# Performance work log

Hardware: AMD Instinct MI355X
Metric: run time of the kernel (lower is better)

Reference implementation:

```python
import jax, jax.numpy as jnp
import numpy as np

TEMPERATURE = 0.07
EPS = 1e-12  # F.normalize eps


def _l2_normalize(x):
    # matches torch F.normalize(dim=1): x / max(||x||, eps)
    n = jnp.linalg.norm(x, axis=1, keepdims=True)
    return x / jnp.maximum(n, EPS)


def setup_inputs() -> dict:
    key = jax.random.key(0)
    k1, k2 = jax.random.split(key)
    N, Z = 4096, 256
    z1 = jax.random.normal(k1, (N, Z), dtype=jnp.float32)
    z2 = jax.random.normal(k2, (N, Z), dtype=jnp.float32)
    return {"z1": z1, "z2": z2}


def reference(z1, z2):
    N = z1.shape[0]
    z1n = _l2_normalize(z1)
    z2n = _l2_normalize(z2)
    reps = jnp.concatenate([z1n, z2n], axis=0)          # [2N, Z]
    sim = reps @ reps.T                                  # cosine sim (rows unit-norm)
    # positives: sim[i, i+N] for i<N and sim[i, i-N] for i>=N
    pos = jnp.concatenate([jnp.diagonal(sim, offset=N),
                           jnp.diagonal(sim, offset=-N)])  # [2N]
    # The row logits are {positive} U {all sims except self and positive},
    # i.e. all entries except the self-similarity diagonal.
    inv_t = 1.0 / TEMPERATURE
    twoN = 2 * N
    diag_mask = jnp.eye(twoN, dtype=bool)
    logits = jnp.where(diag_mask, -jnp.inf, sim * inv_t)   # [2N, 2N]
    lse = jax.nn.logsumexp(logits, axis=1)                 # [2N]
    # cross_entropy with label at the positive: -pos/T + lse, sum / 2N
    loss = jnp.mean(lse - pos * inv_t)
    return loss
```

## Files before the change

### kernel.cpp

```cpp
#include <hip/hip_runtime.h>
#include <hip/hip_bf16.h>

#define N_ROWS 4096
#define TWO_N  8192
#define ZDIM   256
#define INV_T  (1.0f/0.07f)
#define EXP_SCALE (INV_T * 1.44269504088896340736f)

typedef __attribute__((ext_vector_type(4))) float f32x4;
typedef __attribute__((ext_vector_type(8))) int   i32x8;
typedef __attribute__((ext_vector_type(2))) int   i32x2;

#define SCALE_ONE 0x7F7F7F7F

__device__ __forceinline__ void async_load16(const void* g, void* lds_uniform_base) {
  __builtin_amdgcn_global_load_lds(
      (const __attribute__((address_space(1))) void*)g,
      (__attribute__((address_space(3))) void*)lds_uniform_base, 16, 0, 0);
}

__device__ __forceinline__ unsigned char f32_to_e4m3(float x) {
  unsigned int u = __float_as_uint(x);
  const unsigned int s = u >> 31;
  unsigned int a = u & 0x7FFFFFFFu;
  if (a > 0x43E00000u) a = 0x43E00000u;
  const float f = __uint_as_float(a);
  unsigned int out;
  if (a < (121u << 23)) {
    const int m = (int)rintf(f * 512.0f);
    out = (unsigned int)m;
  } else {
    const unsigned int r = a + 0x7FFFFu + ((a >> 20) & 1u);
    const unsigned int e8 = (r >> 23) - 120u;
    out = (e8 << 3) | ((r >> 20) & 7u);
  }
  return (unsigned char)(out | (s << 7));
}

__global__ __launch_bounds__(256) void normalize_kernel(
    const float* __restrict__ z1, const float* __restrict__ z2,
    unsigned char* __restrict__ reps, float* __restrict__ pos,
    float* __restrict__ out) {
  const int lane = threadIdx.x & 63;
  const int wave = threadIdx.x >> 6;
  const int r = blockIdx.x * 4 + wave;
  const float4 a = ((const float4*)(z1 + (size_t)r * ZDIM))[lane];
  const float4 b = ((const float4*)(z2 + (size_t)r * ZDIM))[lane];
  float s1 = a.x*a.x + a.y*a.y + a.z*a.z + a.w*a.w;
  float s2 = b.x*b.x + b.y*b.y + b.z*b.z + b.w*b.w;
  float s3 = a.x*b.x + a.y*b.y + a.z*b.z + a.w*b.w;
  #pragma unroll
  for (int m = 1; m < 64; m <<= 1) {
    s1 += __shfl_xor(s1, m, 64);
    s2 += __shfl_xor(s2, m, 64);
    s3 += __shfl_xor(s3, m, 64);
  }
  const float inv1 = 1.0f / fmaxf(sqrtf(s1), 1e-12f);
  const float inv2 = 1.0f / fmaxf(sqrtf(s2), 1e-12f);
  uchar4 pa, pb;
  pa.x = f32_to_e4m3(a.x * inv1); pa.y = f32_to_e4m3(a.y * inv1);
  pa.z = f32_to_e4m3(a.z * inv1); pa.w = f32_to_e4m3(a.w * inv1);
  pb.x = f32_to_e4m3(b.x * inv2); pb.y = f32_to_e4m3(b.y * inv2);
  pb.z = f32_to_e4m3(b.z * inv2); pb.w = f32_to_e4m3(b.w * inv2);
  ((uchar4*)(reps + (size_t)r * ZDIM))[lane] = pa;
  ((uchar4*)(reps + (size_t)(r + N_ROWS) * ZDIM))[lane] = pb;
  if (lane == 0) {
    pos[r] = s3 * inv1 * inv2;
    if (r == 0) out[0] = INV_T;
  }
}

__global__ __launch_bounds__(256, 2) void simsum_kernel(
    const unsigned char* __restrict__ reps,
    float* __restrict__ rowscratch,
    float* __restrict__ colscratch) {
  __shared__ __align__(16) unsigned char Alds[128 * 256];
  __shared__ __align__(16) unsigned char Blds[2][128 * 128];
  __shared__ float colred[2][256];

  const int tid  = threadIdx.x;
  const int lane = tid & 63;
  const int wave = tid >> 6;
  const int wm = wave >> 1, wn = wave & 1;
  const int quad = lane >> 4;
  const int l16  = lane & 15;
  const int itile = blockIdx.x;
  const int chunk = blockIdx.y;
  const int rowBase = itile * 128;
  const char* gbase = (const char*)reps;
  const bool diaghere = (chunk == 0);

  {
    const int r0 = tid >> 4;
    const int src = (tid & 8) | ((tid ^ (tid >> 4)) & 7);
    const char* g0 = gbase + (rowBase + r0) * ZDIM + src * 16;
    char* l0 = (char*)Alds + (wave << 10);
    #pragma unroll
    for (int p = 0; p < 8; ++p)
      async_load16(g0 + p * 16 * ZDIM, l0 + p * 4096);
  }

  int doff[4];
  int noff;
  if (diaghere) {
    doff[0] = 1; doff[1] = 2; doff[2] = 3; doff[3] = 32;
    noff = (itile < 32) ? 4 : 3;
  } else {
    doff[0] = chunk * 4; doff[1] = chunk * 4 + 1;
    doff[2] = chunk * 4 + 2; doff[3] = chunk * 4 + 3;
    noff = 4;
  }
  const int Q = noff * 2;

#define STAGE_B(q_) do {                                                        \
    const int t_ = (q_) >> 1, c_ = (q_) & 1;                                    \
    const int jt_ = (itile + doff[t_]) & 63;                                    \
    const int r0_ = tid >> 3;                                        \
    const int src_ = (tid ^ (tid >> 3)) & 7;                                    \
    const char* g0_ = gbase + (jt_ * 128 + r0_) * ZDIM + c_ * 128 + src_ * 16;  \
    char* l0_ = (char*)Blds[c_] + (wave << 10);                                 \
    _Pragma("unroll")                                                           \
    for (int p_ = 0; p_ < 4; ++p_)                                              \
      async_load16(g0_ + p_ * 32 * ZDIM, l0_ + p_ * 4096);                      \
  } while (0)

  float rowpart[16];
  #pragma unroll
  for (int i = 0; i < 16; ++i) rowpart[i] = 0.0f;
  const f32x4 zero4 = {0.0f, 0.0f, 0.0f, 0.0f};

  if (diaghere) {
    __syncthreads();
    if (Q > 0) STAGE_B(0);
    f32x4 acc[4][4];
    #pragma unroll
    for (int mi = 0; mi < 4; ++mi)
      #pragma unroll
      for (int ni = 0; ni < 4; ++ni) acc[mi][ni] = zero4;
    #pragma unroll
    for (int h = 0; h < 2; ++h) {
      i32x8 afrag[4], bfrag[4];
      #pragma unroll
      for (int mi = 0; mi < 4; ++mi) {
        const int m = wm * 64 + mi * 16 + l16;
        #pragma unroll
        for (int ws = 0; ws < 4; ++ws) {
          const int o = h * 16 + ws * 4 + quad;
          const int k16 = o >> 1, half = (o & 1) * 8;
          const int sw = (k16 & 8) | ((k16 ^ m) & 7);
          const i32x2 t = *(const i32x2*)((const char*)Alds + m * 256 + sw * 16 + half);
          afrag[mi][2 * ws] = t.x; afrag[mi][2 * ws + 1] = t.y;
        }
      }
      #pragma unroll
      for (int ni = 0; ni < 4; ++ni) {
        const int n = wn * 64 + ni * 16 + l16;
        #pragma unroll
        for (int ws = 0; ws < 4; ++ws) {
          const int o = h * 16 + ws * 4 + quad;
          const int k16 = o >> 1, half = (o & 1) * 8;
          const int sw = (k16 & 8) | ((k16 ^ n) & 7);
          const i32x2 t = *(const i32x2*)((const char*)Alds + n * 256 + sw * 16 + half);
          bfrag[ni][2 * ws] = t.x; bfrag[ni][2 * ws + 1] = t.y;
        }
      }
      #pragma unroll
      for (int mi = 0; mi < 4; ++mi)
        #pragma unroll
        for (int ni = 0; ni < 4; ++ni)
          acc[mi][ni] = __builtin_amdgcn_mfma_scale_f32_16x16x128_f8f6f4(
              afrag[mi], bfrag[ni], acc[mi][ni], 0, 0,
              0, SCALE_ONE, 0, SCALE_ONE);
    }
    #pragma unroll
    for (int mi = 0; mi < 4; ++mi)
      #pragma unroll
      for (int r = 0; r < 4; ++r) {
        const int grow = rowBase + wm * 64 + mi * 16 + quad * 4 + r;
        float s = 0.0f;
        #pragma unroll
        for (int ni = 0; ni < 4; ++ni) {
          const int gcol = rowBase + wn * 64 + ni * 16 + l16;
          const float e = exp2f((acc[mi][ni][r] - 1.0f) * EXP_SCALE);
          if (grow != gcol) s += e;
        }
        rowpart[mi * 4 + r] += s;
      }
    __syncthreads();
  } else {
    STAGE_B(0);
    __syncthreads();
  }

  f32x4 acc[4][4];
  for (int q = 0; q < Q; ++q) {
    if (q + 1 < Q) STAGE_B(q + 1);
    const int t = q >> 1, c = q & 1;
    const int d = doff[t];
    const int jtile = (itile + d) & 63;

    if (c == 0) {
      #pragma unroll
      for (int mi = 0; mi < 4; ++mi)
        #pragma unroll
        for (int ni = 0; ni < 4; ++ni) acc[mi][ni] = zero4;
    }
    {
      i32x8 afrag[4], bfrag[4];
      #pragma unroll
      for (int mi = 0; mi < 4; ++mi) {
        const int m = wm * 64 + mi * 16 + l16;
        #pragma unroll
        for (int ws = 0; ws < 4; ++ws) {
          const int o = c * 16 + ws * 4 + quad;
          const int k16 = o >> 1, half = (o & 1) * 8;
          const int sw = (k16 & 8) | ((k16 ^ m) & 7);
          const i32x2 t = *(const i32x2*)((const char*)Alds + m * 256 + sw * 16 + half);
          afrag[mi][2 * ws] = t.x; afrag[mi][2 * ws + 1] = t.y;
        }
      }
      #pragma unroll
      for (int ni = 0; ni < 4; ++ni) {
        const int n = wn * 64 + ni * 16 + l16;
        #pragma unroll
        for (int ws = 0; ws < 4; ++ws) {
          const int ol = ws * 4 + quad;
          const int k16l = ol >> 1, halfl = (ol & 1) * 8;
          const int sw = (k16l ^ n) & 7;
          const i32x2 t = *(const i32x2*)((const char*)Blds[c] + n * 128 + sw * 16 + halfl);
          bfrag[ni][2 * ws] = t.x; bfrag[ni][2 * ws + 1] = t.y;
        }
      }
      #pragma unroll
      for (int mi = 0; mi < 4; ++mi)
        #pragma unroll
        for (int ni = 0; ni < 4; ++ni)
          acc[mi][ni] = __builtin_amdgcn_mfma_scale_f32_16x16x128_f8f6f4(
              afrag[mi], bfrag[ni], acc[mi][ni], 0, 0,
              0, SCALE_ONE, 0, SCALE_ONE);
    }

    if (c == 1) {
      float colpart[4] = {0.0f, 0.0f, 0.0f, 0.0f};
      #pragma unroll
      for (int mi = 0; mi < 4; ++mi)
        #pragma unroll
        for (int r = 0; r < 4; ++r) {
          float s = 0.0f;
          #pragma unroll
          for (int ni = 0; ni < 4; ++ni) {
            const float e = exp2f((acc[mi][ni][r] - 1.0f) * EXP_SCALE);
            s += e;
            colpart[ni] += e;
          }
          rowpart[mi * 4 + r] += s;
        }
      #pragma unroll
      for (int ni = 0; ni < 4; ++ni) {
        float v = colpart[ni];
        v += __shfl_xor(v, 16, 64);
        v += __shfl_xor(v, 32, 64);
        if (quad == 0) colred[t & 1][wm * 128 + wn * 64 + ni * 16 + l16] = v;
      }
      __syncthreads();
      if (tid < 128)
        colscratch[(jtile * 32 + (d - 1)) * 128 + tid] =
            colred[t & 1][tid] + colred[t & 1][128 + tid];
    } else {
      __syncthreads();
    }
  }

  #pragma unroll
  for (int i = 0; i < 16; ++i) {
    float v = rowpart[i];
    v += __shfl_xor(v, 1, 64);
    v += __shfl_xor(v, 2, 64);
    v += __shfl_xor(v, 4, 64);
    v += __shfl_xor(v, 8, 64);
    rowpart[i] = v;
  }
  __syncthreads();
  if (l16 == 0) {
    #pragma unroll
    for (int mi = 0; mi < 4; ++mi)
      #pragma unroll
      for (int r = 0; r < 4; ++r)
        colred[0][wn * 128 + wm * 64 + mi * 16 + quad * 4 + r] = rowpart[mi * 4 + r];
  }
  __syncthreads();
  if (tid < 128)
    rowscratch[(itile * 8 + chunk) * 128 + tid] = colred[0][tid] + colred[0][128 + tid];
#undef STAGE_B
}

__global__ __launch_bounds__(256) void reduce_kernel(
    const float* __restrict__ rowscratch, const float* __restrict__ colscratch,
    const float* __restrict__ pos, float* __restrict__ out) {
  const int bid = blockIdx.x;
  const int tid = threadIdx.x;
  const int j  = bid * 16 + (tid >> 4);
  const int k  = tid & 15;
  const int jt = j >> 7, o = j & 127;
  const int ns = (jt < 32) ? 31 : 32;
  const int limit = 8 + ns;
  float s = 0.0f;
  #pragma unroll
  for (int step = 0; step < 3; ++step) {
    const int idx = k + step * 16;
    if (idx < limit)
      s += (idx < 8) ? rowscratch[(jt * 8 + idx) * 128 + o]
                     : colscratch[(jt * 32 + (idx - 8)) * 128 + o];
  }
  s += __shfl_xor(s, 1, 64);
  s += __shfl_xor(s, 2, 64);
  s += __shfl_xor(s, 4, 64);
  s += __shfl_xor(s, 8, 64);
  float v = (k == 0) ? logf(s) * (1.0f / (float)TWO_N) : 0.0f;
  if (tid < 8) v -= pos[bid * 8 + tid] * (INV_T / (float)N_ROWS);
  #pragma unroll
  for (int m = 1; m < 64; m <<= 1) v += __shfl_xor(v, m, 64);
  __shared__ float red[4];
  if ((tid & 63) == 0) red[tid >> 6] = v;
  __syncthreads();
  if (tid == 0) atomicAdd(out, red[0] + red[1] + red[2] + red[3]);
}

extern "C" void kernel_launch(void* const* d_in, const int* in_sizes, int n_in,
                              void* d_out, int out_size, void* d_ws, size_t ws_size,
                              hipStream_t stream) {
  const float* z1 = (const float*)d_in[0];
  const float* z2 = (const float*)d_in[1];
  char* ws = (char*)d_ws;
  unsigned char* reps = (unsigned char*)ws;
  size_t off = (size_t)TWO_N * ZDIM;
  float* pos = (float*)(ws + off);        off += N_ROWS * 4;
  float* rowscratch = (float*)(ws + off); off += 64 * 8 * 128 * 4;
  float* colscratch = (float*)(ws + off); off += 64 * 32 * 128 * 4;

  normalize_kernel<<<1024, 256, 0, stream>>>(z1, z2, reps, pos, (float*)d_out);
  simsum_kernel<<<dim3(64, 8), 256, 0, stream>>>(reps, rowscratch, colscratch);
  reduce_kernel<<<512, 256, 0, stream>>>(rowscratch, colscratch, pos, (float*)d_out);
}
```

Measured before the change: 94.96 us.

## Keep A fragments in registers and unroll B K-halves with explicit double buffering

The A tile fragments for both K halves are now loaded from LDS into registers once per block, instead of being reloaded for every B tile and half. The inner loop now runs over tiles with two explicit K-half stages, so each B half-buffer can be prefetched while the other is consumed. This removes repeated LDS reads and the loop-control branching on the half index. In exchange, 64 extra VGPRs are held for A, which raises register pressure and may lower occupancy.

```diff
diff --git a/kernel.cpp b/kernel.cpp
--- a/kernel.cpp
+++ b/kernel.cpp
@@ -110,20 +110,38 @@
     doff[2] = chunk * 4 + 2; doff[3] = chunk * 4 + 3;
     noff = 4;
   }
-  const int Q = noff * 2;
-
-#define STAGE_B(q_) do {                                                        \
-    const int t_ = (q_) >> 1, c_ = (q_) & 1;                                    \
+
+#define STAGE_B2(t_, c_) do {                                                   \
     const int jt_ = (itile + doff[t_]) & 63;                                    \
     const int r0_ = tid >> 3;                                        \
     const int src_ = (tid ^ (tid >> 3)) & 7;                                    \
-    const char* g0_ = gbase + (jt_ * 128 + r0_) * ZDIM + c_ * 128 + src_ * 16;  \
+    const char* g0_ = gbase + (jt_ * 128 + r0_) * ZDIM + (c_) * 128 + src_ * 16;\
     char* l0_ = (char*)Blds[c_] + (wave << 10);                                 \
     _Pragma("unroll")                                                           \
     for (int p_ = 0; p_ < 4; ++p_)                                              \
       async_load16(g0_ + p_ * 32 * ZDIM, l0_ + p_ * 4096);                      \
   } while (0)
 
+  i32x8 areg[4][2];
+#define LOAD_AREG() do {                                                        \
+    _Pragma("unroll")                                                           \
+    for (int mi = 0; mi < 4; ++mi) {                                            \
+      const int m_ = wm * 64 + mi * 16 + l16;                                   \
+      _Pragma("unroll")                                                         \
+      for (int cc = 0; cc < 2; ++cc) {                                          \
+        _Pragma("unroll")                                                       \
+        for (int ws = 0; ws < 4; ++ws) {                                        \
+          const int o_ = cc * 16 + ws * 4 + quad;                               \
+          const int k16_ = o_ >> 1, half_ = (o_ & 1) * 8;                       \
+          const int sw_ = (k16_ & 8) | ((k16_ ^ m_) & 7);                       \
+          const i32x2 tt_ = *(const i32x2*)((const char*)Alds + m_ * 256 +      \
+                                            sw_ * 16 + half_);                  \
+          areg[mi][cc][2 * ws] = tt_.x; areg[mi][cc][2 * ws + 1] = tt_.y;       \
+        }                                                                       \
+      }                                                                         \
+    }                                                                           \
+  } while (0)
+
   float rowpart[16];
   #pragma unroll
   for (int i = 0; i < 16; ++i) rowpart[i] = 0.0f;
@@ -131,7 +149,8 @@
 
   if (diaghere) {
     __syncthreads();
-    if (Q > 0) STAGE_B(0);
+    STAGE_B2(0, 0);
+    LOAD_AREG();
     f32x4 acc[4][4];
     #pragma unroll
     for (int mi = 0; mi < 4; ++mi)
@@ -139,19 +158,7 @@
       for (int ni = 0; ni < 4; ++ni) acc[mi][ni] = zero4;
     #pragma unroll
     for (int h = 0; h < 2; ++h) {
-      i32x8 afrag[4], bfrag[4];
-      #pragma unroll
-      for (int mi = 0; mi < 4; ++mi) {
-        const int m = wm * 64 + mi * 16 + l16;
-        #pragma unroll
-        for (int ws = 0; ws < 4; ++ws) {
-          const int o = h * 16 + ws * 4 + quad;
-          const int k16 = o >> 1, half = (o & 1) * 8;
-          const int sw = (k16 & 8) | ((k16 ^ m) & 7);
-          const i32x2 t = *(const i32x2*)((const char*)Alds + m * 256 + sw * 16 + half);
-          afrag[mi][2 * ws] = t.x; afrag[mi][2 * ws + 1] = t.y;
-        }
-      }
+      i32x8 bfrag[4];
       #pragma unroll
       for (int ni = 0; ni < 4; ++ni) {
         const int n = wn * 64 + ni * 16 + l16;
@@ -169,7 +176,7 @@
         #pragma unroll
         for (int ni = 0; ni < 4; ++ni)
           acc[mi][ni] = __builtin_amdgcn_mfma_scale_f32_16x16x128_f8f6f4(
-              afrag[mi], bfrag[ni], acc[mi][ni], 0, 0,
+              areg[mi][h], bfrag[ni], acc[mi][ni], 0, 0,
               0, SCALE_ONE, 0, SCALE_ONE);
     }
     #pragma unroll
@@ -188,59 +195,52 @@
       }
     __syncthreads();
   } else {
-    STAGE_B(0);
+    STAGE_B2(0, 0);
     __syncthreads();
-  }
+    LOAD_AREG();
+  }
+
+#define COMPUTE_HALF(CC) do {                                                   \
+    i32x8 bfrag[4];                                                             \
+    _Pragma("unroll")                                                           \
+    for (int ni = 0; ni < 4; ++ni) {                                            \
+      const int n = wn * 64 + ni * 16 + l16;                                    \
+      _Pragma("unroll")                                                         \
+      for (int ws = 0; ws < 4; ++ws) {                                          \
+        const int ol = ws * 4 + quad;                    \
+        const int k16l = ol >> 1, halfl = (ol & 1) * 8;                         \
+        const int sw = (k16l ^ n) & 7;                                          \
+        const i32x2 t = *(const i32x2*)((const char*)Blds[CC] + n * 128 +       \
+                                        sw * 16 + halfl);                       \
+        bfrag[ni][2 * ws] = t.x; bfrag[ni][2 * ws + 1] = t.y;                   \
+      }                                                                         \
+    }                                                                           \
+    _Pragma("unroll")                                                           \
+    for (int mi = 0; mi < 4; ++mi)                                              \
+      _Pragma("unroll")                                                         \
+      for (int ni = 0; ni < 4; ++ni)                                            \
+        acc[mi][ni] = __builtin_amdgcn_mfma_scale_f32_16x16x128_f8f6f4(         \
+            areg[mi][CC], bfrag[ni], acc[mi][ni], 0, 0,                         \
+            0, SCALE_ONE, 0, SCALE_ONE);                                        \
+  } while (0)
 
   f32x4 acc[4][4];
-  for (int q = 0; q < Q; ++q) {
-    if (q + 1 < Q) STAGE_B(q + 1);
-    const int t = q >> 1, c = q & 1;
+  for (int t = 0; t < noff; ++t) {
     const int d = doff[t];
     const int jtile = (itile + d) & 63;
 
-    if (c == 0) {
-      #pragma unroll
-      for (int mi = 0; mi < 4; ++mi)
-        #pragma unroll
-        for (int ni = 0; ni < 4; ++ni) acc[mi][ni] = zero4;
-    }
+    STAGE_B2(t, 1);
+    #pragma unroll
+    for (int mi = 0; mi < 4; ++mi)
+      #pragma unroll
+      for (int ni = 0; ni < 4; ++ni) acc[mi][ni] = zero4;
+    COMPUTE_HALF(0);
+    __syncthreads();
+
+    if (t + 1 < noff) STAGE_B2(t + 1, 0);
+    COMPUTE_HALF(1);
+
     {
-      i32x8 afrag[4], bfrag[4];
-      #pragma unroll
-      for (int mi = 0; mi < 4; ++mi) {
-        const int m = wm * 64 + mi * 16 + l16;
-        #pragma unroll
-        for (int ws = 0; ws < 4; ++ws) {
-          const int o = c * 16 + ws * 4 + quad;
-          const int k16 = o >> 1, half = (o & 1) * 8;
-          const int sw = (k16 & 8) | ((k16 ^ m) & 7);
-          const i32x2 t = *(const i32x2*)((const char*)Alds + m * 256 + sw * 16 + half);
-          afrag[mi][2 * ws] = t.x; afrag[mi][2 * ws + 1] = t.y;
-        }
-      }
-      #pragma unroll
-      for (int ni = 0; ni < 4; ++ni) {
-        const int n = wn * 64 + ni * 16 + l16;
-        #pragma unroll
-        for (int ws = 0; ws < 4; ++ws) {
-          const int ol = ws * 4 + quad;
-          const int k16l = ol >> 1, halfl = (ol & 1) * 8;
-          const int sw = (k16l ^ n) & 7;
-          const i32x2 t = *(const i32x2*)((const char*)Blds[c] + n * 128 + sw * 16 + halfl);
-          bfrag[ni][2 * ws] = t.x; bfrag[ni][2 * ws + 1] = t.y;
-        }
-      }
-      #pragma unroll
-      for (int mi = 0; mi < 4; ++mi)
-        #pragma unroll
-        for (int ni = 0; ni < 4; ++ni)
-          acc[mi][ni] = __builtin_amdgcn_mfma_scale_f32_16x16x128_f8f6f4(
-              afrag[mi], bfrag[ni], acc[mi][ni], 0, 0,
-              0, SCALE_ONE, 0, SCALE_ONE);
-    }
-
-    if (c == 1) {
       float colpart[4] = {0.0f, 0.0f, 0.0f, 0.0f};
       #pragma unroll
       for (int mi = 0; mi < 4; ++mi)
@@ -266,8 +266,6 @@
       if (tid < 128)
         colscratch[(jtile * 32 + (d - 1)) * 128 + tid] =
             colred[t & 1][tid] + colred[t & 1][128 + tid];
-    } else {
-      __syncthreads();
     }
   }
 
@@ -291,7 +289,9 @@
   __syncthreads();
   if (tid < 128)
     rowscratch[(itile * 8 + chunk) * 128 + tid] = colred[0][tid] + colred[0][128 + tid];
-#undef STAGE_B
+#undef STAGE_B2
+#undef LOAD_AREG
+#undef COMPUTE_HALF
 }
 
 __global__ __launch_bounds__(256) void reduce_kernel(
```

After: 93.72 us. About the same (-1.3%).
